# Kernel tuning notes

Hardware: AMD Instinct MI355X
Metric: run time of the kernel (lower is better)

The kernel has to match this reference:

```python
import jax, jax.numpy as jnp
import numpy as np

SOS = 1
H = 1024
E = 512
V = 32000


def setup_inputs() -> dict:
    key = jax.random.key(0)
    ks = jax.random.split(key, 16)
    B, T_enc, T = 32, 128, 64
    s = 1.0 / np.sqrt(H)
    inp = {
        'encoder_outputs': jax.random.normal(ks[0], (B, T_enc, H), jnp.float32),
        'encoder_hidden': jax.random.normal(ks[1], (1, B, H), jnp.float32),
        'encoder_cell': jax.random.normal(ks[2], (1, B, H), jnp.float32),
        'target_tensor': jax.random.randint(ks[3], (B, T), 0, V),
        'emb_table': jax.random.normal(ks[4], (V, E), jnp.float32) * 0.02,
        'Wa': jax.random.normal(ks[5], (H, H), jnp.float32) * s,
        'Ua': jax.random.normal(ks[6], (H, H), jnp.float32) * s,
        'Va_w': jax.random.normal(ks[7], (1, H), jnp.float32) * s,
        'Va_b': jnp.zeros((1,), jnp.float32),
        'W_ih': jax.random.normal(ks[8], (4 * H, E + H), jnp.float32) * s,
        'W_hh': jax.random.normal(ks[9], (4 * H, H), jnp.float32) * s,
        'b_ih': jnp.zeros((4 * H,), jnp.float32),
        'b_hh': jnp.zeros((4 * H,), jnp.float32),
        'fc_w': jax.random.normal(ks[10], (V, H), jnp.float32) * s,
        'fc_b': jnp.zeros((V,), jnp.float32),
    }
    return inp


def reference(encoder_outputs, encoder_hidden, encoder_cell, target_tensor,
              emb_table, Wa, Ua, Va_w, Va_b, W_ih, W_hh, b_ih, b_hh, fc_w, fc_b):
    B, T = target_tensor.shape
    # padding_idx=0: embedding row 0 is zeros
    emb_table = emb_table.at[0].set(0.0)
    enc_Ua = jnp.einsum('bth,kh->btk', encoder_outputs, Ua)  # precompute Ua(enc)
    # teacher forcing always: inputs are [SOS, target[:, :-1]], shape [T, B]
    tok_seq = jnp.concatenate([jnp.full((B, 1), SOS, target_tensor.dtype),
                               target_tensor[:, :-1]], axis=1).T

    def step(carry, tok):
        h, c = carry  # [B, H]
        emb = emb_table[tok]  # [B, E]
        # Bahdanau attention (query = last-layer hidden)
        q = h @ Wa.T  # [B, H]
        energy = jnp.tanh(q[:, None, :] + enc_Ua)  # [B, T_enc, H]
        scores = jnp.einsum('bth,h->bt', energy, Va_w[0]) + Va_b[0]
        w = jax.nn.softmax(scores, axis=1)
        context = jnp.einsum('bt,bth->bh', w, encoder_outputs)
        x = jnp.concatenate([emb, context], axis=1)  # [B, E+H]
        gates = x @ W_ih.T + b_ih + h @ W_hh.T + b_hh  # [B, 4H], order i,f,g,o
        i, f, g, o = jnp.split(gates, 4, axis=1)
        c = jax.nn.sigmoid(f) * c + jax.nn.sigmoid(i) * jnp.tanh(g)
        h = jax.nn.sigmoid(o) * jnp.tanh(c)
        logp = jax.nn.log_softmax(h @ fc_w.T + fc_b, axis=1)  # [B, V]
        return (h, c), logp

    (h, c), logps = jax.lax.scan(step, (encoder_hidden[0], encoder_cell[0]), tok_seq)
    outputs = jnp.transpose(logps, (1, 0, 2))  # [B, T, V]
    return outputs
```

## Files before the change

kernel.cpp:

```cpp
#include <hip/hip_runtime.h>
#include <math.h>

#define NB 32
#define TE 128
#define NT 64
#define HH 1024
#define EE 512
#define VV 32000
#define GG 4096
#define WQN 5120
#define NBLK 512

typedef __attribute__((ext_vector_type(8))) short bh8;
typedef __attribute__((ext_vector_type(4))) float fx4;
typedef __attribute__((ext_vector_type(4))) unsigned ux4;
typedef __attribute__((ext_vector_type(4))) float fv4;
typedef __attribute__((ext_vector_type(2))) float fv2;

__device__ __forceinline__ float tanh_fast(float x) {
  float e = __expf(2.f * x);
  return 1.f - 2.f / (e + 1.f);
}
__device__ __forceinline__ float sigf(float x) { return 1.f / (1.f + __expf(-x)); }
__device__ __forceinline__ ushort f2bf(float x) {
  union { float f; unsigned u; } v; v.f = x;
  unsigned r = v.u + 0x7fffu + ((v.u >> 16) & 1u);
  return (ushort)(r >> 16);
}
__device__ __forceinline__ float bf2f(ushort u) {
  return __uint_as_float(((unsigned)u) << 16);
}

__device__ __forceinline__ void st_f32(float* p, float v) {
  __hip_atomic_store(p, v, __ATOMIC_RELAXED, __HIP_MEMORY_SCOPE_AGENT);
}
__device__ __forceinline__ float ld_f32(const float* p) {
  return __hip_atomic_load(p, __ATOMIC_RELAXED, __HIP_MEMORY_SCOPE_AGENT);
}
__device__ __forceinline__ void st_u32(unsigned* p, unsigned v) {
  __hip_atomic_store(p, v, __ATOMIC_RELAXED, __HIP_MEMORY_SCOPE_AGENT);
}
__device__ __forceinline__ unsigned ld_u32(const unsigned* p) {
  return __hip_atomic_load(p, __ATOMIC_RELAXED, __HIP_MEMORY_SCOPE_AGENT);
}

__global__ void k_init(const float* __restrict__ eh, unsigned* __restrict__ h_u32) {
  int i = blockIdx.x * 256 + threadIdx.x;
  float a = eh[i * 2], b = eh[i * 2 + 1];
  h_u32[i] = (unsigned)f2bf(a) | ((unsigned)f2bf(b) << 16);
}

__global__ void k_emb(const int* __restrict__ tgt, const float* __restrict__ etab,
                      ushort* __restrict__ emb_bf) {
  int idx = blockIdx.x * 256 + threadIdx.x;
  int e = idx & (EE - 1);
  int tb = idx >> 9;
  int b = tb & (NB - 1);
  int t = tb >> 5;
  int tok = (t == 0) ? 1 : tgt[b * NT + (t - 1)];
  emb_bf[idx] = (tok == 0) ? (ushort)0 : f2bf(etab[(size_t)tok * EE + e]);
}

__global__ void k_f2b(const float* __restrict__ s, ushort* __restrict__ d, int n4) {
  int i = blockIdx.x * 256 + threadIdx.x;
  if (i >= n4) return;
  float4 v = *(const float4*)(s + (size_t)i * 4);
  *(ushort4*)(d + (size_t)i * 4) = make_ushort4(f2bf(v.x), f2bf(v.y), f2bf(v.z), f2bf(v.w));
}

__global__ void k_f2b_s(const float* __restrict__ s, int ld, int off, int w4,
                        ushort* __restrict__ d, int n) {
  int i = blockIdx.x * 256 + threadIdx.x;
  if (i >= n) return;
  int r = i / w4, c = (i - r * w4) * 4;
  float4 v = *(const float4*)(s + (size_t)r * ld + off + c);
  *(ushort4*)(d + (size_t)r * (w4 * 4) + c) = make_ushort4(f2bf(v.x), f2bf(v.y), f2bf(v.z), f2bf(v.w));
}

__device__ __forceinline__ void stage_pair(const ushort* A, int lda, const ushort* B, int ldb,
    int m0, int n0, int k0, ushort* ldsA, ushort* ldsB, int tid) {
  const int w = tid >> 6;
  const int row = tid >> 2;
  const int kq = (tid & 3) * 8;
  const ushort* ga = A + (size_t)(m0 + row) * lda + k0 + kq;
  const ushort* gb = B + (size_t)(n0 + row) * ldb + k0 + kq;
  ushort* la = ldsA + w * 512;
  ushort* lb = ldsB + w * 512;
  __builtin_amdgcn_global_load_lds((const __attribute__((address_space(1))) void*)ga,
      (__attribute__((address_space(3))) void*)la, 16, 0, 0);
  __builtin_amdgcn_global_load_lds((const __attribute__((address_space(1))) void*)(ga + (size_t)64 * lda),
      (__attribute__((address_space(3))) void*)(la + 2048), 16, 0, 0);
  __builtin_amdgcn_global_load_lds((const __attribute__((address_space(1))) void*)gb,
      (__attribute__((address_space(3))) void*)lb, 16, 0, 0);
  __builtin_amdgcn_global_load_lds((const __attribute__((address_space(1))) void*)(gb + (size_t)64 * ldb),
      (__attribute__((address_space(3))) void*)(lb + 2048), 16, 0, 0);
}

__global__ __launch_bounds__(256) void k_gemm_bf16(
    const ushort* __restrict__ A, int lda,
    const ushort* __restrict__ B, int ldb,
    const float* __restrict__ b1, const float* __restrict__ b2,
    void* __restrict__ Cv, int ldc, int K, int perm, int obf, int swz) {
  __shared__ ushort lds[2][2][4096];
  const int tid = threadIdx.x;
  const int lane = tid & 63, w = tid >> 6;
  int m0, n0;
  if (swz) {
    const int bid = blockIdx.y * gridDim.x + blockIdx.x;
    m0 = (bid & 15) * 128;
    n0 = (bid >> 4) * 128;
  } else {
    m0 = blockIdx.y * 128;
    n0 = blockIdx.x * 128;
  }
  const int wm = (w >> 1) * 64, wn = (w & 1) * 64;
  fx4 acc[4][4] = {};
  stage_pair(A, lda, B, ldb, m0, n0, 0, lds[0][0], lds[0][1], tid);
  __syncthreads();
  const int nk = K >> 5;
  const int ko = (lane >> 4) * 8;
  const int rA = wm + (lane & 15);
  const int rB = wn + (lane & 15);
  for (int ks = 0; ks < nk; ++ks) {
    const int cur = ks & 1;
    if (ks + 1 < nk)
      stage_pair(A, lda, B, ldb, m0, n0, (ks + 1) << 5, lds[cur ^ 1][0], lds[cur ^ 1][1], tid);
    bh8 af[4], bfr[4];
#pragma unroll
    for (int f = 0; f < 4; ++f) {
      af[f]  = *(const bh8*)(&lds[cur][0][(rA + f * 16) * 32 + ko]);
      bfr[f] = *(const bh8*)(&lds[cur][1][(rB + f * 16) * 32 + ko]);
    }
#pragma unroll
    for (int i = 0; i < 4; ++i)
#pragma unroll
      for (int j = 0; j < 4; ++j)
        acc[i][j] = __builtin_amdgcn_mfma_f32_16x16x32_bf16(af[i], bfr[j], acc[i][j], 0, 0, 0);
    __syncthreads();
  }
  float* Cf = (float*)Cv;
  ushort* Cb = (ushort*)Cv;
#pragma unroll
  for (int j = 0; j < 4; ++j) {
    const int col = n0 + wn + j * 16 + (lane & 15);
    const float bv = (b1 ? b1[col] : 0.f) + (b2 ? b2[col] : 0.f);
#pragma unroll
    for (int i = 0; i < 4; ++i) {
      const int mb = m0 + wm + i * 16 + (lane >> 4) * 4;
#pragma unroll
      for (int r = 0; r < 4; ++r) {
        const int m = mb + r;
        const size_t orow = perm ? ((size_t)(m & 31) * 64 + (m >> 5)) : (size_t)m;
        const float v = acc[i][j][r] + bv;
        if (obf) Cb[orow * (size_t)ldc + col] = f2bf(v);
        else     Cf[orow * (size_t)ldc + col] = v;
      }
    }
  }
}

__device__ __forceinline__ void gridbar(unsigned* flags, unsigned* gen, unsigned epoch) {
  asm volatile("s_waitcnt vmcnt(0)" ::: "memory");
  __syncthreads();
  const int tid = threadIdx.x;
  if (tid == 0) st_u32(flags + blockIdx.x * 32, epoch);
  if (blockIdx.x == 0) {
    while (ld_u32(flags + tid * 32) < epoch) __builtin_amdgcn_s_sleep(1);
    while (ld_u32(flags + (256 + tid) * 32) < epoch) __builtin_amdgcn_s_sleep(1);
    __syncthreads();
    if (tid == 0) st_u32(gen, epoch);
  } else if (tid == 0) {
    while (ld_u32(gen) < epoch) __builtin_amdgcn_s_sleep(1);
  }
  __syncthreads();
}

__global__ __launch_bounds__(256, 1) void k_recur(
    const ushort* __restrict__ Wqh,
    const ushort* __restrict__ encU,
    const ushort* __restrict__ encW,
    const float*  __restrict__ embG,
    const float*  __restrict__ Va,
    const float*  __restrict__ ec,
    float* __restrict__ hW,
    float* __restrict__ sc,
    unsigned* __restrict__ h_u32,
    ushort* __restrict__ hall,
    unsigned* __restrict__ flags, unsigned* __restrict__ gen) {
  const int bid = blockIdx.x;
  const int tid = threadIdx.x;
  const int lane = tid & 63, w = tid >> 6;
  __shared__ float wlds[4][32][33];
  __shared__ float red[128], wt[TE], gp[4][64];
  unsigned epoch = 0;

  const int b3 = bid >> 4, u0 = (bid & 15) * 64;
  float c0r = 0.f, c1r = 0.f;
  if (tid < 32) {
    c0r = ec[b3 * HH + u0 + tid * 2];
    c1r = ec[b3 * HH + u0 + tid * 2 + 1];
  }
  const int bb = bid >> 4, tc = bid & 15;

  for (int t = 0; t < NT; ++t) {
    if (bid < 160) {
      const int n0 = bid * 32;
      const int kb = w * 256;
      const int r15 = lane & 15, ko = (lane >> 4) * 8;
      const char* hbase0 = (const char*)h_u32 + r15 * 2048 + (size_t)(kb + ko) * 2;
      const char* hbase1 = hbase0 + 16 * 2048;
      const ushort* B0 = Wqh + (size_t)(n0 + r15) * HH + kb + ko;
      const ushort* B1 = B0 + 16 * HH;
      fx4 a00 = {}, a01 = {}, a10 = {}, a11 = {};
#pragma unroll
      for (int half = 0; half < 2; ++half) {
        union { ux4 u; bh8 b; } h0[4], h1[4];
        const char* p0 = hbase0 + half * 256;
        const char* p1 = hbase1 + half * 256;
        asm volatile(
          "global_load_dwordx4 %0, %8, off sc0 sc1\n\t"
          "global_load_dwordx4 %1, %8, off offset:64 sc0 sc1\n\t"
          "global_load_dwordx4 %2, %8, off offset:128 sc0 sc1\n\t"
          "global_load_dwordx4 %3, %8, off offset:192 sc0 sc1\n\t"
          "global_load_dwordx4 %4, %9, off sc0 sc1\n\t"
          "global_load_dwordx4 %5, %9, off offset:64 sc0 sc1\n\t"
          "global_load_dwordx4 %6, %9, off offset:128 sc0 sc1\n\t"
          "global_load_dwordx4 %7, %9, off offset:192 sc0 sc1\n\t"
          "s_waitcnt vmcnt(0)"
          : "=&v"(h0[0].u), "=&v"(h0[1].u), "=&v"(h0[2].u), "=&v"(h0[3].u),
            "=&v"(h1[0].u), "=&v"(h1[1].u), "=&v"(h1[2].u), "=&v"(h1[3].u)
          : "v"(p0), "v"(p1));
#pragma unroll
        for (int ks = 0; ks < 4; ++ks) {
          const int k = (half * 4 + ks) * 32;
          bh8 bv0 = *(const bh8*)(B0 + k);
          bh8 bv1 = *(const bh8*)(B1 + k);
          a00 = __builtin_amdgcn_mfma_f32_16x16x32_bf16(h0[ks].b, bv0, a00, 0, 0, 0);
          a01 = __builtin_amdgcn_mfma_f32_16x16x32_bf16(h0[ks].b, bv1, a01, 0, 0, 0);
          a10 = __builtin_amdgcn_mfma_f32_16x16x32_bf16(h1[ks].b, bv0, a10, 0, 0, 0);
          a11 = __builtin_amdgcn_mfma_f32_16x16x32_bf16(h1[ks].b, bv1, a11, 0, 0, 0);
        }
      }
      const int rr = (lane >> 4) * 4;
#pragma unroll
      for (int r = 0; r < 4; ++r) {
        wlds[w][rr + r][r15]           = a00[r];
        wlds[w][rr + r][r15 + 16]      = a01[r];
        wlds[w][16 + rr + r][r15]      = a10[r];
        wlds[w][16 + rr + r][r15 + 16] = a11[r];
      }
      __syncthreads();
      const int row = tid >> 3, c0 = (tid & 7) * 4;
      fv4 s4;
      s4.x = wlds[0][row][c0+0] + wlds[1][row][c0+0] + wlds[2][row][c0+0] + wlds[3][row][c0+0];
      s4.y = wlds[0][row][c0+1] + wlds[1][row][c0+1] + wlds[2][row][c0+1] + wlds[3][row][c0+1];
      s4.z = wlds[0][row][c0+2] + wlds[1][row][c0+2] + wlds[2][row][c0+2] + wlds[3][row][c0+2];
      s4.w = wlds[0][row][c0+3] + wlds[1][row][c0+3] + wlds[2][row][c0+3] + wlds[3][row][c0+3];
      asm volatile("global_store_dwordx4 %0, %1, off sc0 sc1"
                   :: "v"(&hW[row * WQN + n0 + c0]), "v"(s4) : "memory");
    }
    gridbar(flags, gen, ++epoch);

    {
      union { ux4 u; float f[4]; } q0, q1, q2, q3;
      const float* qp0 = &hW[bb * WQN + lane * 8];
      const float* qp1 = &hW[bb * WQN + 512 + lane * 8];
      asm volatile(
        "global_load_dwordx4 %0, %4, off sc0 sc1\n\t"
        "global_load_dwordx4 %1, %4, off offset:16 sc0 sc1\n\t"
        "global_load_dwordx4 %2, %5, off sc0 sc1\n\t"
        "global_load_dwordx4 %3, %5, off offset:16 sc0 sc1\n\t"
        "s_waitcnt vmcnt(0)"
        : "=&v"(q0.u), "=&v"(q1.u), "=&v"(q2.u), "=&v"(q3.u)
        : "v"(qp0), "v"(qp1));
      float qr[16], vr[16];
#pragma unroll
      for (int j = 0; j < 4; ++j) {
        qr[j] = q0.f[j]; qr[4 + j] = q1.f[j];
        qr[8 + j] = q2.f[j]; qr[12 + j] = q3.f[j];
      }
#pragma unroll
      for (int c = 0; c < 2; ++c) {
        const int h0 = c * 512 + lane * 8;
        float4 va = *(const float4*)(Va + h0);
        float4 vb = *(const float4*)(Va + h0 + 4);
        vr[c*8+0] = va.x; vr[c*8+1] = va.y; vr[c*8+2] = va.z; vr[c*8+3] = va.w;
        vr[c*8+4] = vb.x; vr[c*8+5] = vb.y; vr[c*8+6] = vb.z; vr[c*8+7] = vb.w;
      }
#pragma unroll
      for (int it = 0; it < 2; ++it) {
        const int tt = tc * 8 + w * 2 + it;
        const ushort* ep = encU + (size_t)(bb * TE + tt) * HH;
        float a = 0.f;
#pragma unroll
        for (int c = 0; c < 2; ++c) {
          bh8 e8 = *(const bh8*)(ep + c * 512 + lane * 8);
#pragma unroll
          for (int j = 0; j < 8; ++j)
            a += tanh_fast(qr[c * 8 + j] + bf2f((ushort)e8[j])) * vr[c * 8 + j];
        }
#pragma unroll
        for (int s2 = 32; s2 > 0; s2 >>= 1) a += __shfl_xor(a, s2);
        if (lane == 0) st_f32(&sc[bb * TE + tt], a);
      }
    }
    gridbar(flags, gen, ++epoch);

    {
      const float sv = (tid < TE) ? ld_f32(&sc[b3 * TE + tid]) : -1e30f;
      if (tid < 128) red[tid] = sv;
      __syncthreads();
      for (int st = 64; st > 0; st >>= 1) {
        if (tid < st) red[tid] = fmaxf(red[tid], red[tid + st]);
        __syncthreads();
      }
      const float mx = red[0];
      __syncthreads();
      const float ev = (tid < TE) ? __expf(sv - mx) : 0.f;
      if (tid < 128) { wt[tid] = ev; red[tid] = ev; }
      __syncthreads();
      for (int st = 64; st > 0; st >>= 1) {
        if (tid < st) red[tid] += red[tid + st];
        __syncthreads();
      }
      const float inv = 1.f / red[0];
      __syncthreads();
      const int p = tid >> 1, th = tid & 1;
      const int g = p >> 5, up = (p & 31) * 2;
      const int col = g * HH + u0 + up;
      const ushort* base = encW + (size_t)(b3 * TE + th * 64) * GG + col;
      float a0 = 0.f, a1 = 0.f;
#pragma unroll 8
      for (int q = 0; q < 64; ++q) {
        ushort2 e2 = *(const ushort2*)(base + (size_t)q * GG);
        const float wv = wt[th * 64 + q];
        a0 += wv * bf2f(e2.x);
        a1 += wv * bf2f(e2.y);
      }
      a0 += __shfl_xor(a0, 1);
      a1 += __shfl_xor(a1, 1);
      if (th == 0) {
        fv2 hv;
        asm volatile("global_load_dwordx2 %0, %1, off sc0 sc1\n\ts_waitcnt vmcnt(0)"
                     : "=&v"(hv) : "v"(&hW[b3 * WQN + HH + col]));
        float2 eg = *(const float2*)(embG + (size_t)(t * NB + b3) * GG + col);
        gp[g][up]     = a0 * inv + eg.x + hv.x;
        gp[g][up + 1] = a1 * inv + eg.y + hv.y;
      }
      __syncthreads();
      if (tid < 32) {
        const int e0 = tid * 2, e1 = tid * 2 + 1;
        const float cn0 = sigf(gp[1][e0]) * c0r + sigf(gp[0][e0]) * tanh_fast(gp[2][e0]);
        const float cn1 = sigf(gp[1][e1]) * c1r + sigf(gp[0][e1]) * tanh_fast(gp[2][e1]);
        c0r = cn0; c1r = cn1;
        const float hn0 = sigf(gp[3][e0]) * tanh_fast(cn0);
        const float hn1 = sigf(gp[3][e1]) * tanh_fast(cn1);
        const ushort hb0 = f2bf(hn0), hb1 = f2bf(hn1);
        st_u32(&h_u32[b3 * 512 + u0 / 2 + tid], (unsigned)hb0 | ((unsigned)hb1 << 16));
        *(ushort2*)(hall + (size_t)t * (NB * HH) + b3 * HH + u0 + e0) = make_ushort2(hb0, hb1);
      }
    }
    gridbar(flags, gen, ++epoch);
  }
}

__global__ __launch_bounds__(256) void k_logsoftmax(float* __restrict__ out) {
  const size_t row = blockIdx.x;
  float* p = out + row * VV;
  __shared__ float sm[256], ss[256];
  const int tid = threadIdx.x;
  float m = -1e30f, s = 0.f;
  for (int i = tid; i < (VV / 4); i += 256) {
    float4 x = *(const float4*)(p + (size_t)i * 4);
    float m4 = fmaxf(fmaxf(x.x, x.y), fmaxf(x.z, x.w));
    float nm = fmaxf(m, m4);
    s = s * __expf(m - nm) + __expf(x.x - nm) + __expf(x.y - nm)
        + __expf(x.z - nm) + __expf(x.w - nm);
    m = nm;
  }
  sm[tid] = m; ss[tid] = s;
  __syncthreads();
  for (int st = 128; st > 0; st >>= 1) {
    if (tid < st) {
      float m2 = fmaxf(sm[tid], sm[tid + st]);
      ss[tid] = ss[tid] * __expf(sm[tid] - m2) + ss[tid + st] * __expf(sm[tid + st] - m2);
      sm[tid] = m2;
    }
    __syncthreads();
  }
  float L = sm[0] + logf(ss[0]);
  __syncthreads();
  for (int i = tid; i < (VV / 4); i += 256) {
    float4 x = *(const float4*)(p + (size_t)i * 4);
    x.x -= L; x.y -= L; x.z -= L; x.w -= L;
    *(float4*)(p + (size_t)i * 4) = x;
  }
}

extern "C" void kernel_launch(void* const* d_in, const int* in_sizes, int n_in,
                              void* d_out, int out_size, void* d_ws, size_t ws_size,
                              hipStream_t stream) {
  const float* enc   = (const float*)d_in[0];
  const float* ehid  = (const float*)d_in[1];
  const float* ecell = (const float*)d_in[2];
  const int*   tgt   = (const int*)d_in[3];
  const float* etab  = (const float*)d_in[4];
  const float* Wa    = (const float*)d_in[5];
  const float* Ua    = (const float*)d_in[6];
  const float* Va_w  = (const float*)d_in[7];
  const float* W_ih  = (const float*)d_in[9];
  const float* W_hh  = (const float*)d_in[10];
  const float* b_ih  = (const float*)d_in[11];
  const float* b_hh  = (const float*)d_in[12];
  const float* fc_w  = (const float*)d_in[13];
  const float* fc_b  = (const float*)d_in[14];
  float* out = (float*)d_out;
  float* ws = (float*)d_ws;

  ushort* encW_bf = (ushort*)ws;
  float*  embG    = ws + 8388608;
  ushort* fcw_bf  = (ushort*)ws;
  ushort* Wqh_bf  = (ushort*)(ws + 16777216);
  ushort* encU_bf = (ushort*)(ws + 19398656);
  ushort* enc_bf  = (ushort*)(ws + 21495808);
  ushort* Wihc_bf = (ushort*)(ws + 23592960);
  ushort* Ua_bf   = (ushort*)(ws + 25690112);
  ushort* emb_bf  = (ushort*)(ws + 26214400);
  ushort* WihE_bf = (ushort*)(ws + 26738688);
  float*  hW      = ws + 21495808;
  float*  sc      = ws + 21659648;
  unsigned* h_u32 = (unsigned*)(ws + 21663744);
  unsigned* flags = (unsigned*)(ws + 27000000);
  unsigned* gen   = (unsigned*)(ws + 27016384);
  ushort* hall_bf = (ushort*)(ws + 27787264);

  k_emb<<<4096, 256, 0, stream>>>(tgt, etab, emb_bf);
  k_f2b<<<4096, 256, 0, stream>>>(enc, enc_bf, 1048576);
  k_f2b<<<1024, 256, 0, stream>>>(Ua, Ua_bf, 262144);
  k_f2b<<<1024, 256, 0, stream>>>(Wa, Wqh_bf, 262144);
  k_f2b<<<4096, 256, 0, stream>>>(W_hh, Wqh_bf + 1024 * HH, 1048576);
  k_f2b_s<<<4096, 256, 0, stream>>>(W_ih, 1536, 512, 256, Wihc_bf, 1048576);
  k_f2b_s<<<2048, 256, 0, stream>>>(W_ih, 1536, 0, 128, WihE_bf, 524288);
  k_gemm_bf16<<<dim3(8, 32), 256, 0, stream>>>(enc_bf, HH, Ua_bf, HH, nullptr, nullptr,
                                               encU_bf, HH, HH, 0, 1, 0);
  k_gemm_bf16<<<dim3(32, 32), 256, 0, stream>>>(enc_bf, HH, Wihc_bf, HH, nullptr, nullptr,
                                                encW_bf, GG, HH, 0, 1, 0);
  k_gemm_bf16<<<dim3(32, 16), 256, 0, stream>>>(emb_bf, EE, WihE_bf, EE, b_ih, b_hh,
                                                embG, GG, EE, 0, 0, 0);
  (void)hipMemsetAsync(flags, 0, (NBLK * 32 + 32) * sizeof(unsigned), stream);
  k_init<<<64, 256, 0, stream>>>(ehid, h_u32);

  k_recur<<<NBLK, 256, 0, stream>>>(Wqh_bf, encU_bf, encW_bf, embG, Va_w, ecell,
                                    hW, sc, h_u32, hall_bf, flags, gen);

  k_f2b<<<32000, 256, 0, stream>>>(fc_w, fcw_bf, 8192000);
  k_gemm_bf16<<<dim3(250, 16), 256, 0, stream>>>(hall_bf, HH, fcw_bf, HH, fc_b, nullptr,
                                                 out, VV, HH, 1, 0, 1);
  k_logsoftmax<<<2048, 256, 0, stream>>>(out);
}
```

Baseline: 1.906 ms.

## Compute attention context directly and apply W_ih context GEMM per step

The precomputed enc×W_ih_context product (B×T_enc×4H bf16) is dropped. Each step now computes the attention context (B×H) from bf16 encoder outputs, then multiplies it by the context slice of W_ih with MFMA in a new phase before the LSTM cell update. This removes a large precompute GEMM and cuts the per-step streaming from a 4H-wide tensor down to H-wide. The cost is an extra grid barrier per step and a bf16 rounding of the context. The grid-barrier release flag is also split into 16 cache-line-separated copies to reduce polling contention.

Measured after the change: 2.090 ms. 1.1x slower.

```diff
diff --git a/kernel.cpp b/kernel.cpp
--- a/kernel.cpp
+++ b/kernel.cpp
@@ -159,7 +159,7 @@
   }
 }
 
-__device__ __forceinline__ void gridbar(unsigned* flags, unsigned* gen, unsigned epoch) {
+__device__ __forceinline__ void gridbar(unsigned* flags, unsigned* genArr, unsigned epoch) {
   asm volatile("s_waitcnt vmcnt(0)" ::: "memory");
   __syncthreads();
   const int tid = threadIdx.x;
@@ -168,9 +168,9 @@
     while (ld_u32(flags + tid * 32) < epoch) __builtin_amdgcn_s_sleep(1);
     while (ld_u32(flags + (256 + tid) * 32) < epoch) __builtin_amdgcn_s_sleep(1);
     __syncthreads();
-    if (tid == 0) st_u32(gen, epoch);
+    if (tid < 16) st_u32(genArr + tid * 32, epoch);
   } else if (tid == 0) {
-    while (ld_u32(gen) < epoch) __builtin_amdgcn_s_sleep(1);
+    while (ld_u32(genArr + (blockIdx.x & 15) * 32) < epoch) __builtin_amdgcn_s_sleep(1);
   }
   __syncthreads();
 }
@@ -178,29 +178,31 @@
 __global__ __launch_bounds__(256, 1) void k_recur(
     const ushort* __restrict__ Wqh,
     const ushort* __restrict__ encU,
-    const ushort* __restrict__ encW,
+    const ushort* __restrict__ encB,
+    const ushort* __restrict__ Wihc,
     const float*  __restrict__ embG,
     const float*  __restrict__ Va,
     const float*  __restrict__ ec,
     float* __restrict__ hW,
     float* __restrict__ sc,
     unsigned* __restrict__ h_u32,
+    unsigned* __restrict__ ctx_u32,
     ushort* __restrict__ hall,
-    unsigned* __restrict__ flags, unsigned* __restrict__ gen) {
+    unsigned* __restrict__ flags, unsigned* __restrict__ genArr) {
   const int bid = blockIdx.x;
   const int tid = threadIdx.x;
   const int lane = tid & 63, w = tid >> 6;
   __shared__ float wlds[4][32][33];
-  __shared__ float red[128], wt[TE], gp[4][64];
+  __shared__ float red[128], wt[TE];
+  __shared__ float cpart[4][16][9];
+  __shared__ float gp2[32][33];
   unsigned epoch = 0;
 
-  const int b3 = bid >> 4, u0 = (bid & 15) * 64;
-  float c0r = 0.f, c1r = 0.f;
-  if (tid < 32) {
-    c0r = ec[b3 * HH + u0 + tid * 2];
-    c1r = ec[b3 * HH + u0 + tid * 2 + 1];
-  }
+  const int uD = bid * 8;
+  float c_r = 0.f;
+  if (bid < 128) c_r = ec[(tid >> 3) * HH + uD + (tid & 7)];
   const int bb = bid >> 4, tc = bid & 15;
+  const int bC = bid >> 3, kc = bid & 7;
 
   for (int t = 0; t < NT; ++t) {
     if (bid < 160) {
@@ -259,7 +261,7 @@
       asm volatile("global_store_dwordx4 %0, %1, off sc0 sc1"
                    :: "v"(&hW[row * WQN + n0 + c0]), "v"(s4) : "memory");
     }
-    gridbar(flags, gen, ++epoch);
+    gridbar(flags, genArr, ++epoch);
 
     {
       union { ux4 u; float f[4]; } q0, q1, q2, q3;
@@ -304,10 +306,10 @@
         if (lane == 0) st_f32(&sc[bb * TE + tt], a);
       }
     }
-    gridbar(flags, gen, ++epoch);
-
-    {
-      const float sv = (tid < TE) ? ld_f32(&sc[b3 * TE + tid]) : -1e30f;
+    gridbar(flags, genArr, ++epoch);
+
+    if (bid < 256) {
+      const float sv = (tid < TE) ? ld_f32(&sc[bC * TE + tid]) : -1e30f;
       if (tid < 128) red[tid] = sv;
       __syncthreads();
       for (int st = 64; st > 0; st >>= 1) {
@@ -325,42 +327,120 @@
       }
       const float inv = 1.f / red[0];
       __syncthreads();
-      const int p = tid >> 1, th = tid & 1;
-      const int g = p >> 5, up = (p & 31) * 2;
-      const int col = g * HH + u0 + up;
-      const ushort* base = encW + (size_t)(b3 * TE + th * 64) * GG + col;
-      float a0 = 0.f, a1 = 0.f;
-#pragma unroll 8
-      for (int q = 0; q < 64; ++q) {
-        ushort2 e2 = *(const ushort2*)(base + (size_t)q * GG);
-        const float wv = wt[th * 64 + q];
-        a0 += wv * bf2f(e2.x);
-        a1 += wv * bf2f(e2.y);
-      }
-      a0 += __shfl_xor(a0, 1);
-      a1 += __shfl_xor(a1, 1);
-      if (th == 0) {
-        fv2 hv;
-        asm volatile("global_load_dwordx2 %0, %1, off sc0 sc1\n\ts_waitcnt vmcnt(0)"
-                     : "=&v"(hv) : "v"(&hW[b3 * WQN + HH + col]));
-        float2 eg = *(const float2*)(embG + (size_t)(t * NB + b3) * GG + col);
-        gp[g][up]     = a0 * inv + eg.x + hv.x;
-        gp[g][up + 1] = a1 * inv + eg.y + hv.y;
-      }
-      __syncthreads();
-      if (tid < 32) {
-        const int e0 = tid * 2, e1 = tid * 2 + 1;
-        const float cn0 = sigf(gp[1][e0]) * c0r + sigf(gp[0][e0]) * tanh_fast(gp[2][e0]);
-        const float cn1 = sigf(gp[1][e1]) * c1r + sigf(gp[0][e1]) * tanh_fast(gp[2][e1]);
-        c0r = cn0; c1r = cn1;
-        const float hn0 = sigf(gp[3][e0]) * tanh_fast(cn0);
-        const float hn1 = sigf(gp[3][e1]) * tanh_fast(cn1);
-        const ushort hb0 = f2bf(hn0), hb1 = f2bf(hn1);
-        st_u32(&h_u32[b3 * 512 + u0 / 2 + tid], (unsigned)hb0 | ((unsigned)hb1 << 16));
-        *(ushort2*)(hall + (size_t)t * (NB * HH) + b3 * HH + u0 + e0) = make_ushort2(hb0, hb1);
-      }
-    }
-    gridbar(flags, gen, ++epoch);
+      const int oct = tid & 15, tg = tid >> 4;
+      const ushort* baseE = encB + (size_t)(bC * TE + tg * 8) * HH + kc * 128 + oct * 8;
+      float a8[8] = {};
+#pragma unroll
+      for (int j = 0; j < 8; ++j) {
+        bh8 e8 = *(const bh8*)(baseE + (size_t)j * HH);
+        const float wv = wt[tg * 8 + j];
+#pragma unroll
+        for (int q = 0; q < 8; ++q) a8[q] += wv * bf2f((ushort)e8[q]);
+      }
+#pragma unroll
+      for (int q = 0; q < 8; ++q) {
+        a8[q] += __shfl_xor(a8[q], 16);
+        a8[q] += __shfl_xor(a8[q], 32);
+      }
+      if (lane < 16) {
+#pragma unroll
+        for (int q = 0; q < 8; ++q) cpart[w][lane][q] = a8[q];
+      }
+      __syncthreads();
+      if (tid < 64) {
+        const int o = tid >> 2, q0 = (tid & 3) * 2;
+        float v0 = (cpart[0][o][q0]   + cpart[1][o][q0])
+                 + (cpart[2][o][q0]   + cpart[3][o][q0]);
+        float v1 = (cpart[0][o][q0+1] + cpart[1][o][q0+1])
+                 + (cpart[2][o][q0+1] + cpart[3][o][q0+1]);
+        v0 *= inv; v1 *= inv;
+        st_u32(&ctx_u32[bC * 512 + kc * 64 + tid],
+               (unsigned)f2bf(v0) | ((unsigned)f2bf(v1) << 16));
+      }
+    }
+    gridbar(flags, genArr, ++epoch);
+
+    if (bid < 128) {
+      const int kb = w * 256;
+      const int r15 = lane & 15, ko = (lane >> 4) * 8;
+      const char* cbase0 = (const char*)ctx_u32 + r15 * 2048 + (size_t)(kb + ko) * 2;
+      const char* cbase1 = cbase0 + 16 * 2048;
+      const ushort* B0 = Wihc + (size_t)((r15 >> 3) * 1024 + uD + (r15 & 7)) * HH + kb + ko;
+      const ushort* B1 = B0 + (size_t)2048 * HH;
+      fx4 a00 = {}, a01 = {}, a10 = {}, a11 = {};
+#pragma unroll
+      for (int half = 0; half < 2; ++half) {
+        union { ux4 u; bh8 b; } h0[4], h1[4];
+        const char* p0 = cbase0 + half * 256;
+        const char* p1 = cbase1 + half * 256;
+        asm volatile(
+          "global_load_dwordx4 %0, %8, off sc0 sc1\n\t"
+          "global_load_dwordx4 %1, %8, off offset:64 sc0 sc1\n\t"
+          "global_load_dwordx4 %2, %8, off offset:128 sc0 sc1\n\t"
+          "global_load_dwordx4 %3, %8, off offset:192 sc0 sc1\n\t"
+          "global_load_dwordx4 %4, %9, off sc0 sc1\n\t"
+          "global_load_dwordx4 %5, %9, off offset:64 sc0 sc1\n\t"
+          "global_load_dwordx4 %6, %9, off offset:128 sc0 sc1\n\t"
+          "global_load_dwordx4 %7, %9, off offset:192 sc0 sc1\n\t"
+          "s_waitcnt vmcnt(0)"
+          : "=&v"(h0[0].u), "=&v"(h0[1].u), "=&v"(h0[2].u), "=&v"(h0[3].u),
+            "=&v"(h1[0].u), "=&v"(h1[1].u), "=&v"(h1[2].u), "=&v"(h1[3].u)
+          : "v"(p0), "v"(p1));
+#pragma unroll
+        for (int ks = 0; ks < 4; ++ks) {
+          const int k = (half * 4 + ks) * 32;
+          bh8 bv0 = *(const bh8*)(B0 + k);
+          bh8 bv1 = *(const bh8*)(B1 + k);
+          a00 = __builtin_amdgcn_mfma_f32_16x16x32_bf16(h0[ks].b, bv0, a00, 0, 0, 0);
+          a01 = __builtin_amdgcn_mfma_f32_16x16x32_bf16(h0[ks].b, bv1, a01, 0, 0, 0);
+          a10 = __builtin_amdgcn_mfma_f32_16x16x32_bf16(h1[ks].b, bv0, a10, 0, 0, 0);
+          a11 = __builtin_amdgcn_mfma_f32_16x16x32_bf16(h1[ks].b, bv1, a11, 0, 0, 0);
+        }
+      }
+      const int rr = (lane >> 4) * 4;
+#pragma unroll
+      for (int r = 0; r < 4; ++r) {
+        wlds[w][rr + r][r15]           = a00[r];
+        wlds[w][rr + r][r15 + 16]      = a01[r];
+        wlds[w][16 + rr + r][r15]      = a10[r];
+        wlds[w][16 + rr + r][r15 + 16] = a11[r];
+      }
+      __syncthreads();
+      {
+        const int row = tid >> 3, c0 = (tid & 7) * 4;
+        const int g = c0 >> 3, uu = uD + (c0 & 7);
+        float4 eg = *(const float4*)(embG + (size_t)(t * NB + row) * GG + g * 1024 + uu);
+        fv4 hv;
+        asm volatile("global_load_dwordx4 %0, %1, off sc0 sc1\n\ts_waitcnt vmcnt(0)"
+                     : "=&v"(hv) : "v"(&hW[row * WQN + HH + g * 1024 + uu]));
+        gp2[row][c0+0] = wlds[0][row][c0+0] + wlds[1][row][c0+0]
+                       + wlds[2][row][c0+0] + wlds[3][row][c0+0] + eg.x + hv.x;
+        gp2[row][c0+1] = wlds[0][row][c0+1] + wlds[1][row][c0+1]
+                       + wlds[2][row][c0+1] + wlds[3][row][c0+1] + eg.y + hv.y;
+        gp2[row][c0+2] = wlds[0][row][c0+2] + wlds[1][row][c0+2]
+                       + wlds[2][row][c0+2] + wlds[3][row][c0+2] + eg.z + hv.z;
+        gp2[row][c0+3] = wlds[0][row][c0+3] + wlds[1][row][c0+3]
+                       + wlds[2][row][c0+3] + wlds[3][row][c0+3] + eg.w + hv.w;
+      }
+      __syncthreads();
+      {
+        const int b = tid >> 3, ul = tid & 7;
+        const float gi = gp2[b][ul], gf = gp2[b][8 + ul];
+        const float gg = gp2[b][16 + ul], go = gp2[b][24 + ul];
+        const float cn = sigf(gf) * c_r + sigf(gi) * tanh_fast(gg);
+        c_r = cn;
+        const float hn = sigf(go) * tanh_fast(cn);
+        const float hn_p = __shfl_xor(hn, 1);
+        const ushort hb = f2bf(hn);
+        if ((ul & 1) == 0) {
+          const ushort hb1 = f2bf(hn_p);
+          st_u32(&h_u32[b * 512 + ((uD + ul) >> 1)],
+                 (unsigned)hb | ((unsigned)hb1 << 16));
+          *(ushort2*)(hall + (size_t)t * (NB * HH) + b * HH + uD + ul) = make_ushort2(hb, hb1);
+        }
+      }
+    }
+    gridbar(flags, genArr, ++epoch);
   }
 }
 
@@ -417,21 +497,21 @@
   float* out = (float*)d_out;
   float* ws = (float*)d_ws;
 
-  ushort* encW_bf = (ushort*)ws;
+  ushort* fcw_bf  = (ushort*)ws;
   float*  embG    = ws + 8388608;
-  ushort* fcw_bf  = (ushort*)ws;
   ushort* Wqh_bf  = (ushort*)(ws + 16777216);
   ushort* encU_bf = (ushort*)(ws + 19398656);
   ushort* enc_bf  = (ushort*)(ws + 21495808);
   ushort* Wihc_bf = (ushort*)(ws + 23592960);
   ushort* Ua_bf   = (ushort*)(ws + 25690112);
+  float*  hW      = ws + 25690112;
+  float*  sc      = ws + 25853952;
+  unsigned* h_u32 = (unsigned*)(ws + 25858048);
+  unsigned* ctx32 = (unsigned*)(ws + 25874432);
   ushort* emb_bf  = (ushort*)(ws + 26214400);
   ushort* WihE_bf = (ushort*)(ws + 26738688);
-  float*  hW      = ws + 21495808;
-  float*  sc      = ws + 21659648;
-  unsigned* h_u32 = (unsigned*)(ws + 21663744);
-  unsigned* flags = (unsigned*)(ws + 27000000);
-  unsigned* gen   = (unsigned*)(ws + 27016384);
+  unsigned* flags = (unsigned*)(ws + 27300000);
+  unsigned* gen   = (unsigned*)(ws + 27316384);
   ushort* hall_bf = (ushort*)(ws + 27787264);
 
   k_emb<<<4096, 256, 0, stream>>>(tgt, etab, emb_bf);
@@ -443,15 +523,13 @@
   k_f2b_s<<<2048, 256, 0, stream>>>(W_ih, 1536, 0, 128, WihE_bf, 524288);
   k_gemm_bf16<<<dim3(8, 32), 256, 0, stream>>>(enc_bf, HH, Ua_bf, HH, nullptr, nullptr,
                                                encU_bf, HH, HH, 0, 1, 0);
-  k_gemm_bf16<<<dim3(32, 32), 256, 0, stream>>>(enc_bf, HH, Wihc_bf, HH, nullptr, nullptr,
-                                                encW_bf, GG, HH, 0, 1, 0);
   k_gemm_bf16<<<dim3(32, 16), 256, 0, stream>>>(emb_bf, EE, WihE_bf, EE, b_ih, b_hh,
                                                 embG, GG, EE, 0, 0, 0);
-  (void)hipMemsetAsync(flags, 0, (NBLK * 32 + 32) * sizeof(unsigned), stream);
+  (void)hipMemsetAsync(flags, 0, (512 * 32 + 16 * 32) * sizeof(unsigned), stream);
   k_init<<<64, 256, 0, stream>>>(ehid, h_u32);
 
-  k_recur<<<NBLK, 256, 0, stream>>>(Wqh_bf, encU_bf, encW_bf, embG, Va_w, ecell,
-                                    hW, sc, h_u32, hall_bf, flags, gen);
+  k_recur<<<NBLK, 256, 0, stream>>>(Wqh_bf, encU_bf, enc_bf, Wihc_bf, embG, Va_w, ecell,
+                                    hW, sc, h_u32, ctx32, hall_bf, flags, gen);
 
   k_f2b<<<32000, 256, 0, stream>>>(fc_w, fcw_bf, 8192000);
   k_gemm_bf16<<<dim3(250, 16), 256, 0, stream>>>(hall_bf, HH, fcw_bf, HH, fc_b, nullptr,
```

## Replicate grid-barrier release flag and vectorize context-gate accumulation

Applied to the files above, without the earlier changes.

The grid barrier's single generation word is replaced by 16 copies on separate cache lines. Each waiting block polls the copy chosen by its index, so 512 pollers no longer contend on one address. The context-times-W_ih stage now has each thread load 8 bf16 values per row over 16 encoder steps, then reduces the partial sums through shared memory, instead of doing strided 2-element loads over 64 steps. The LSTM cell update is spread over 64 threads and uses a shuffle to pack the bf16 output pairs. The flag region is moved and the memset is enlarged to cover the extra words.

After: 1.900 ms. No clear change (-0.3%).

```diff
diff --git a/kernel.cpp b/kernel.cpp
--- a/kernel.cpp
+++ b/kernel.cpp
@@ -15,7 +15,6 @@
 typedef __attribute__((ext_vector_type(4))) float fx4;
 typedef __attribute__((ext_vector_type(4))) unsigned ux4;
 typedef __attribute__((ext_vector_type(4))) float fv4;
-typedef __attribute__((ext_vector_type(2))) float fv2;
 
 __device__ __forceinline__ float tanh_fast(float x) {
   float e = __expf(2.f * x);
@@ -159,7 +158,7 @@
   }
 }
 
-__device__ __forceinline__ void gridbar(unsigned* flags, unsigned* gen, unsigned epoch) {
+__device__ __forceinline__ void gridbar(unsigned* flags, unsigned* genArr, unsigned epoch) {
   asm volatile("s_waitcnt vmcnt(0)" ::: "memory");
   __syncthreads();
   const int tid = threadIdx.x;
@@ -168,9 +167,9 @@
     while (ld_u32(flags + tid * 32) < epoch) __builtin_amdgcn_s_sleep(1);
     while (ld_u32(flags + (256 + tid) * 32) < epoch) __builtin_amdgcn_s_sleep(1);
     __syncthreads();
-    if (tid == 0) st_u32(gen, epoch);
+    if (tid < 16) st_u32(genArr + tid * 32, epoch);
   } else if (tid == 0) {
-    while (ld_u32(gen) < epoch) __builtin_amdgcn_s_sleep(1);
+    while (ld_u32(genArr + (blockIdx.x & 15) * 32) < epoch) __builtin_amdgcn_s_sleep(1);
   }
   __syncthreads();
 }
@@ -186,20 +185,18 @@
     float* __restrict__ sc,
     unsigned* __restrict__ h_u32,
     ushort* __restrict__ hall,
-    unsigned* __restrict__ flags, unsigned* __restrict__ gen) {
+    unsigned* __restrict__ flags, unsigned* __restrict__ genArr) {
   const int bid = blockIdx.x;
   const int tid = threadIdx.x;
   const int lane = tid & 63, w = tid >> 6;
   __shared__ float wlds[4][32][33];
   __shared__ float red[128], wt[TE], gp[4][64];
+  __shared__ float cpart[8][4][8][8];
   unsigned epoch = 0;
 
   const int b3 = bid >> 4, u0 = (bid & 15) * 64;
-  float c0r = 0.f, c1r = 0.f;
-  if (tid < 32) {
-    c0r = ec[b3 * HH + u0 + tid * 2];
-    c1r = ec[b3 * HH + u0 + tid * 2 + 1];
-  }
+  float c_r = 0.f;
+  if (tid < 64) c_r = ec[b3 * HH + u0 + tid];
   const int bb = bid >> 4, tc = bid & 15;
 
   for (int t = 0; t < NT; ++t) {
@@ -259,7 +256,7 @@
       asm volatile("global_store_dwordx4 %0, %1, off sc0 sc1"
                    :: "v"(&hW[row * WQN + n0 + c0]), "v"(s4) : "memory");
     }
-    gridbar(flags, gen, ++epoch);
+    gridbar(flags, genArr, ++epoch);
 
     {
       union { ux4 u; float f[4]; } q0, q1, q2, q3;
@@ -304,7 +301,7 @@
         if (lane == 0) st_f32(&sc[bb * TE + tt], a);
       }
     }
-    gridbar(flags, gen, ++epoch);
+    gridbar(flags, genArr, ++epoch);
 
     {
       const float sv = (tid < TE) ? ld_f32(&sc[b3 * TE + tid]) : -1e30f;
@@ -325,42 +322,49 @@
       }
       const float inv = 1.f / red[0];
       __syncthreads();
-      const int p = tid >> 1, th = tid & 1;
-      const int g = p >> 5, up = (p & 31) * 2;
-      const int col = g * HH + u0 + up;
-      const ushort* base = encW + (size_t)(b3 * TE + th * 64) * GG + col;
-      float a0 = 0.f, a1 = 0.f;
-#pragma unroll 8
-      for (int q = 0; q < 64; ++q) {
-        ushort2 e2 = *(const ushort2*)(base + (size_t)q * GG);
-        const float wv = wt[th * 64 + q];
-        a0 += wv * bf2f(e2.x);
-        a1 += wv * bf2f(e2.y);
-      }
-      a0 += __shfl_xor(a0, 1);
-      a1 += __shfl_xor(a1, 1);
-      if (th == 0) {
-        fv2 hv;
-        asm volatile("global_load_dwordx2 %0, %1, off sc0 sc1\n\ts_waitcnt vmcnt(0)"
-                     : "=&v"(hv) : "v"(&hW[b3 * WQN + HH + col]));
-        float2 eg = *(const float2*)(embG + (size_t)(t * NB + b3) * GG + col);
-        gp[g][up]     = a0 * inv + eg.x + hv.x;
-        gp[g][up + 1] = a1 * inv + eg.y + hv.y;
-      }
-      __syncthreads();
-      if (tid < 32) {
-        const int e0 = tid * 2, e1 = tid * 2 + 1;
-        const float cn0 = sigf(gp[1][e0]) * c0r + sigf(gp[0][e0]) * tanh_fast(gp[2][e0]);
-        const float cn1 = sigf(gp[1][e1]) * c1r + sigf(gp[0][e1]) * tanh_fast(gp[2][e1]);
-        c0r = cn0; c1r = cn1;
-        const float hn0 = sigf(gp[3][e0]) * tanh_fast(cn0);
-        const float hn1 = sigf(gp[3][e1]) * tanh_fast(cn1);
-        const ushort hb0 = f2bf(hn0), hb1 = f2bf(hn1);
-        st_u32(&h_u32[b3 * 512 + u0 / 2 + tid], (unsigned)hb0 | ((unsigned)hb1 << 16));
-        *(ushort2*)(hall + (size_t)t * (NB * HH) + b3 * HH + u0 + e0) = make_ushort2(hb0, hb1);
-      }
-    }
-    gridbar(flags, gen, ++epoch);
+      const int oct = tid & 7, g = (tid >> 3) & 3, tq = tid >> 5;
+      const ushort* base = encW + (size_t)(b3 * TE + tq * 16) * GG + g * 1024 + u0 + oct * 8;
+      float a8[8] = {};
+#pragma unroll
+      for (int j = 0; j < 16; ++j) {
+        bh8 e8 = *(const bh8*)(base + (size_t)j * GG);
+        const float wv = wt[tq * 16 + j];
+#pragma unroll
+        for (int q = 0; q < 8; ++q) a8[q] += wv * bf2f((ushort)e8[q]);
+      }
+#pragma unroll
+      for (int q = 0; q < 8; ++q) cpart[tq][g][oct][q] = a8[q];
+      __syncthreads();
+      {
+        const int c = tid & 63, g2 = tid >> 6;
+        float s = 0.f;
+#pragma unroll
+        for (int q = 0; q < 8; ++q) s += cpart[q][g2][c >> 3][c & 7];
+        s *= inv;
+        const int cl = g2 * 1024 + u0 + c;
+        s += embG[(size_t)(t * NB + b3) * GG + cl];
+        float hv;
+        asm volatile("global_load_dword %0, %1, off sc0 sc1\n\ts_waitcnt vmcnt(0)"
+                     : "=&v"(hv) : "v"(&hW[b3 * WQN + HH + cl]));
+        gp[g2][c] = s + hv;
+      }
+      __syncthreads();
+      if (tid < 64) {
+        const float gi = gp[0][tid], gf = gp[1][tid];
+        const float gg = gp[2][tid], go = gp[3][tid];
+        const float cn = sigf(gf) * c_r + sigf(gi) * tanh_fast(gg);
+        c_r = cn;
+        const float hn = sigf(go) * tanh_fast(cn);
+        const float hn_p = __shfl_xor(hn, 1);
+        if ((tid & 1) == 0) {
+          const ushort hb = f2bf(hn), hb1 = f2bf(hn_p);
+          st_u32(&h_u32[b3 * 512 + ((u0 + tid) >> 1)],
+                 (unsigned)hb | ((unsigned)hb1 << 16));
+          *(ushort2*)(hall + (size_t)t * (NB * HH) + b3 * HH + u0 + tid) = make_ushort2(hb, hb1);
+        }
+      }
+    }
+    gridbar(flags, genArr, ++epoch);
   }
 }
 
@@ -430,8 +434,8 @@
   float*  hW      = ws + 21495808;
   float*  sc      = ws + 21659648;
   unsigned* h_u32 = (unsigned*)(ws + 21663744);
-  unsigned* flags = (unsigned*)(ws + 27000000);
-  unsigned* gen   = (unsigned*)(ws + 27016384);
+  unsigned* flags = (unsigned*)(ws + 27300000);
+  unsigned* genArr= (unsigned*)(ws + 27316384);
   ushort* hall_bf = (ushort*)(ws + 27787264);
 
   k_emb<<<4096, 256, 0, stream>>>(tgt, etab, emb_bf);
@@ -447,11 +451,11 @@
                                                 encW_bf, GG, HH, 0, 1, 0);
   k_gemm_bf16<<<dim3(32, 16), 256, 0, stream>>>(emb_bf, EE, WihE_bf, EE, b_ih, b_hh,
                                                 embG, GG, EE, 0, 0, 0);
-  (void)hipMemsetAsync(flags, 0, (NBLK * 32 + 32) * sizeof(unsigned), stream);
+  (void)hipMemsetAsync(flags, 0, (NBLK * 32 + 16 * 32) * sizeof(unsigned), stream);
   k_init<<<64, 256, 0, stream>>>(ehid, h_u32);
 
   k_recur<<<NBLK, 256, 0, stream>>>(Wqh_bf, encU_bf, encW_bf, embG, Va_w, ecell,
-                                    hW, sc, h_u32, hall_bf, flags, gen);
+                                    hW, sc, h_u32, hall_bf, flags, genArr);
 
   k_f2b<<<32000, 256, 0, stream>>>(fc_w, fcw_bf, 8192000);
   k_gemm_bf16<<<dim3(250, 16), 256, 0, stream>>>(hall_bf, HH, fcw_bf, HH, fc_b, nullptr,
```
